# Kernel optimization log

Hardware: AMD Instinct MI355X
Metric: run time of the kernel (lower is better)

Reference implementation:

```python
import jax, jax.numpy as jnp
import numpy as np

B = 8192
DIM = 1024
NI = 16
ALPHA = 0.5
BETA = 1.0


def setup_inputs() -> dict:
    key = jax.random.key(0)
    ks = jax.random.split(key, 12)
    d, n = DIM, NI
    din = d + d // n  # local expert input width = 1088
    s = 0.02  # small init scale to keep softplus in a sane range
    return {
        "y": jax.random.normal(ks[0], (B, d), jnp.float32),
        "M": jax.random.normal(ks[1], (B, d), jnp.float32),
        # global discriminator params ([in, out] layout)
        "gw0": jax.random.normal(ks[2], (d, d), jnp.float32) * s,
        "gb0": jnp.zeros((d,), jnp.float32),
        "gw1": jax.random.normal(ks[3], (d, d), jnp.float32) * s,
        "gb1": jnp.zeros((d,), jnp.float32),
        "l0w": jax.random.normal(ks[4], (2 * d, 128), jnp.float32) * s,
        "l0b": jnp.zeros((128,), jnp.float32),
        "l1w": jax.random.normal(ks[5], (128, 128), jnp.float32) * s,
        "l1b": jnp.zeros((128,), jnp.float32),
        "l2w": jax.random.normal(ks[6], (128, 1), jnp.float32) * s,
        "l2b": jnp.zeros((1,), jnp.float32),
        # local discriminator: n_interpretator stacked expert MLPs
        "lW1": jax.random.normal(ks[7], (n, din, 128), jnp.float32) * s,
        "lb1": jnp.zeros((n, 128), jnp.float32),
        "lW2": jax.random.normal(ks[8], (n, 128, 128), jnp.float32) * s,
        "lb2": jnp.zeros((n, 128), jnp.float32),
        "lW3": jax.random.normal(ks[9], (n, 128, 1), jnp.float32) * s,
        "lb3": jnp.zeros((n, 1), jnp.float32),
        "n_interpretator": NI,
    }


def reference(y, M, gw0, gb0, gw1, gb1, l0w, l0b, l1w, l1b, l2w, l2b,
              lW1, lb1, lW2, lb2, lW3, lb3, n_interpretator):
    n = n_interpretator
    Bsz, d = y.shape
    M3 = M.reshape(Bsz, d // n, n)                              # [B, d/n, n]
    Mp3 = jnp.concatenate([M3[1:], M3[:1]], axis=0)             # shuffled negatives
    y_exp = jnp.broadcast_to(y[:, :, None], (Bsz, d, n))        # [B, d, n]
    yM = jnp.concatenate([M3, y_exp], axis=1)                   # [B, d/n + d, n]
    yMp = jnp.concatenate([Mp3, y_exp], axis=1)

    def local_d(x):
        # batched over the n expert groups: grouped GEMMs instead of a loop
        h = jax.nn.relu(jnp.einsum('bdn,ndh->bnh', x, lW1) + lb1)   # [B, n, 128]
        h = jax.nn.relu(jnp.einsum('bnh,nhk->bnk', h, lW2) + lb2)   # [B, n, 128]
        s = jnp.einsum('bnh,nho->bno', h, lW3) + lb3                # [B, n, 1]
        return s[..., 0]                                            # [B, n]

    Ej_l = -jnp.mean(jax.nn.softplus(-local_d(yM)))
    Em_l = jnp.mean(jax.nn.softplus(local_d(yMp)))
    LOCAL = (Em_l - Ej_l) * BETA

    def global_d(yy, Mm):
        h = jax.nn.relu(Mm.reshape(Bsz, -1) @ gw0 + gb0) @ gw1 + gb1  # net(M)
        h = jnp.concatenate([yy, h], axis=1)                          # [B, 2d]
        h = jax.nn.relu(h @ l0w + l0b)
        h = jax.nn.relu(h @ l1w + l1b)
        return h @ l2w + l2b                                          # [B, 1]

    Ej_g = -jnp.mean(jax.nn.softplus(-global_d(y, M3)))
    Em_g = jnp.mean(jax.nn.softplus(global_d(y, Mp3)))
    GLOBAL = (Em_g - Ej_g) * ALPHA

    return LOCAL + GLOBAL
```

## Files before the change

kernel.cpp:

```cpp
#include <hip/hip_runtime.h>
#include <hip/hip_bf16.h>
#include <math.h>

#define B_ROWS 8192
#define NEXP 16

typedef __attribute__((ext_vector_type(8))) short short8;
typedef __attribute__((ext_vector_type(4))) float f32x4;

__device__ __forceinline__ float softplus_f(float x) {
    return fmaxf(x, 0.f) + log1pf(expf(-fabsf(x)));
}

__device__ __forceinline__ float bf2f(short u) {
    union { unsigned int i; float f; } c;
    c.i = ((unsigned int)(unsigned short)u) << 16;
    return c.f;
}

__device__ __forceinline__ short f2bf_s(float x) {
    __hip_bfloat16 h = __float2bfloat16(x);
    return *(short*)&h;
}

__device__ __forceinline__ void gll16(const void* g, void* l) {
    __builtin_amdgcn_global_load_lds(
        (const __attribute__((address_space(1))) void*)g,
        (__attribute__((address_space(3))) void*)l, 16, 0, 0);
}

#define FENCE() asm volatile("" ::: "memory")
#define VM3 asm volatile("s_waitcnt vmcnt(3)" ::: "memory")
#define VM0 asm volatile("s_waitcnt vmcnt(0)" ::: "memory")
#define BAR __builtin_amdgcn_s_barrier()

__global__ __launch_bounds__(256) void prep_all(
    const float* __restrict__ y, const float* __restrict__ M,
    const float* __restrict__ lW1, const float* __restrict__ gw0,
    const float* __restrict__ l0w, const float* __restrict__ gw1,
    __hip_bfloat16* __restrict__ yb, short* __restrict__ Mt2,
    __hip_bfloat16* __restrict__ W1yt, short* __restrict__ W1m2,
    __hip_bfloat16* __restrict__ W0p, __hip_bfloat16* __restrict__ l0wyt,
    float* __restrict__ wgtp)
{
    __shared__ __align__(16) char smem[33280];
    const int b = blockIdx.x;
    const int tid = threadIdx.x;
    const int lane = tid & 63, w = tid >> 6;

    if (b < 64) {
        short* As = (short*)smem;
        short* Bs = (short*)(smem + 16384);
        const int ct = b & 7, ks = b >> 3;
        const int bn = ct * 128;
        const int wr = w >> 1, wc = w & 1;
        const int l15 = lane & 15, l4 = lane >> 4;

        f32x4 acc4[4][4] = {};
        for (int kq = 0; kq < 2; ++kq) {
            const int k0 = ks * 128 + kq * 64;
            {
                int c4 = (tid & 31) * 4;
                int kkr0 = tid >> 5;
                #pragma unroll
                for (int r = 0; r < 8; ++r) {
                    int kk = r * 8 + kkr0;
                    float4 v = *(const float4*)&l0w[(long)(1024 + k0 + kk) * 128 + c4];
                    int g = kk >> 3, sub = kk & 7;
                    #pragma unroll
                    for (int i = 0; i < 4; ++i) {
                        int row = c4 + i;
                        As[row * 64 + (g ^ (row & 7)) * 8 + sub] = f2bf_s(((const float*)&v)[i]);
                    }
                }
            }
            {
                int jr0 = tid >> 3;
                int g = tid & 7;
                #pragma unroll
                for (int s = 0; s < 4; ++s) {
                    int jrel = s * 32 + jr0;
                    const float* src = &gw1[(long)(bn + jrel) * 1024 + k0 + g * 8];
                    float4 v0 = *(const float4*)src;
                    float4 v1 = *(const float4*)(src + 4);
                    union { short8 v; short sh[8]; } o;
                    o.sh[0] = f2bf_s(v0.x); o.sh[1] = f2bf_s(v0.y);
                    o.sh[2] = f2bf_s(v0.z); o.sh[3] = f2bf_s(v0.w);
                    o.sh[4] = f2bf_s(v1.x); o.sh[5] = f2bf_s(v1.y);
                    o.sh[6] = f2bf_s(v1.z); o.sh[7] = f2bf_s(v1.w);
                    *(short8*)&Bs[jrel * 64 + (g ^ (jrel & 7)) * 8] = o.v;
                }
            }
            __syncthreads();
            #pragma unroll
            for (int st = 0; st < 2; ++st) {
                const int gr = (st * 4 + l4) ^ (l15 & 7);
                short8 a[4], bv[4];
                #pragma unroll
                for (int m = 0; m < 4; ++m)
                    a[m] = *(const short8*)&As[(wr * 64 + m * 16 + l15) * 64 + gr * 8];
                #pragma unroll
                for (int n = 0; n < 4; ++n)
                    bv[n] = *(const short8*)&Bs[(wc * 64 + n * 16 + l15) * 64 + gr * 8];
                #pragma unroll
                for (int m = 0; m < 4; ++m)
                    #pragma unroll
                    for (int n = 0; n < 4; ++n)
                        acc4[m][n] = __builtin_amdgcn_mfma_f32_16x16x32_bf16(a[m], bv[n], acc4[m][n], 0, 0, 0);
            }
            __syncthreads();
        }
        #pragma unroll
        for (int m = 0; m < 4; ++m) {
            int row = wr * 64 + m * 16 + l4 * 4;
            #pragma unroll
            for (int n = 0; n < 4; ++n) {
                int col = bn + wc * 64 + n * 16 + l15;
                #pragma unroll
                for (int r = 0; r < 4; ++r)
                    wgtp[((long)ks * 128 + row + r) * 1024 + col] = acc4[m][n][r];
            }
        }
        return;
    }

    if (b < 1088) {
        const long base = (long)(b - 64) * 2048;
        #pragma unroll
        for (int j = 0; j < 8; ++j) {
            long i = base + j * 256 + tid;
            float4 v = ((const float4*)y)[i];
            union { ushort4 u; __hip_bfloat16 h[4]; } p;
            p.h[0] = __float2bfloat16(v.x);
            p.h[1] = __float2bfloat16(v.y);
            p.h[2] = __float2bfloat16(v.z);
            p.h[3] = __float2bfloat16(v.w);
            ((ushort4*)yb)[i] = p.u;
        }
        return;
    }

    if (b < 2112) {
        short* t = (short*)smem;
        const long r0 = (long)(b - 1088) * 8;
        #pragma unroll
        for (int i = 0; i < 8; ++i) {
            int idx = i * 1024 + tid * 4;
            float4 v = *(const float4*)&M[r0 * 1024 + idx];
            short4 s;
            s.x = f2bf_s(v.x); s.y = f2bf_s(v.y); s.z = f2bf_s(v.z); s.w = f2bf_s(v.w);
            *(short4*)&t[idx] = s;
        }
        __syncthreads();
        const int e = tid & 15, rr = (tid >> 4) & 7, hf = tid >> 7;
        #pragma unroll
        for (int c = 0; c < 4; ++c) {
            union { short8 v; short s[8]; } o;
            #pragma unroll
            for (int j = 0; j < 8; ++j)
                o.s[j] = t[rr * 1024 + (hf * 32 + c * 8 + j) * 16 + e];
            *(short8*)&Mt2[(long)(e >> 1) * (8192L * 128) + (r0 + rr) * 128
                           + (e & 1) * 64 + hf * 32 + c * 8] = o.v;
        }
        return;
    }

    float (*t)[129] = (float(*)[129])smem;

    if (b < 2624) {
        int l = b - 2112, bx = l & 15, by = l >> 4;
        int n0 = bx * 128, k0 = by * 32;
        long base = 64L * 128 + (long)bx * (1088L * 128);
        #pragma unroll
        for (int ll = 0; ll < 16; ++ll) {
            int idx = tid + ll * 256;
            int kk = idx >> 7, nn = idx & 127;
            t[kk][nn] = lW1[base + (long)(k0 + kk) * 128 + nn];
        }
        __syncthreads();
        int nn = tid >> 1, kb = (tid & 1) * 16;
        #pragma unroll
        for (int j = 0; j < 16; ++j)
            W1yt[(long)(n0 + nn) * 1024 + k0 + kb + j] = __float2bfloat16(t[kb + j][nn]);
        return;
    }

    if (b < 2656) {
        int l = b - 2624, bx = l & 15, by = l >> 4;
        int n0 = bx * 128, k0 = by * 32;
        long base = (long)bx * (1088L * 128);
        #pragma unroll
        for (int ll = 0; ll < 16; ++ll) {
            int idx = tid + ll * 256;
            int kk = idx >> 7, nn = idx & 127;
            if (kk < 32) t[kk][nn] = lW1[base + (long)(k0 + kk) * 128 + nn];
        }
        __syncthreads();
        int nn = tid >> 1, kb = (tid & 1) * 16;
        int half = bx & 1;
        #pragma unroll
        for (int j = 0; j < 16; ++j) {
            W1m2[(long)(n0 + nn) * 128 + half * 64 + k0 + kb + j] = f2bf_s(t[kb + j][nn]);
            W1m2[(long)(n0 + nn) * 128 + (1 - half) * 64 + k0 + kb + j] = 0;
        }
        return;
    }

    if (b < 2912) {
        int l = b - 2656, bx = l & 7, by = l >> 3;
        int n0 = bx * 128, k0 = by * 32;
        int e = k0 >> 6, dd0 = k0 & 63;
        #pragma unroll
        for (int ll = 0; ll < 16; ++ll) {
            int idx = tid + ll * 256;
            int kk = idx >> 7, nn = idx & 127;
            t[kk][nn] = gw0[(long)((dd0 + kk) * 16 + e) * 1024 + n0 + nn];
        }
        __syncthreads();
        int nn = tid >> 1, kb = (tid & 1) * 16;
        #pragma unroll
        for (int j = 0; j < 16; ++j)
            W0p[(long)(n0 + nn) * 1024 + k0 + kb + j] = __float2bfloat16(t[kb + j][nn]);
        return;
    }

    {
        int by = b - 2912;
        int k0 = by * 32;
        #pragma unroll
        for (int ll = 0; ll < 16; ++ll) {
            int idx = tid + ll * 256;
            int kk = idx >> 7, nn = idx & 127;
            t[kk][nn] = l0w[(long)(k0 + kk) * 128 + nn];
        }
        __syncthreads();
        int nn = tid >> 1, kb = (tid & 1) * 16;
        #pragma unroll
        for (int j = 0; j < 16; ++j)
            l0wyt[(long)nn * 1024 + k0 + kb + j] = __float2bfloat16(t[kb + j][nn]);
        return;
    }
}

__global__ __launch_bounds__(512, 4) void gemm3s(
    const short* __restrict__ yb, const short* __restrict__ W1yt,
    __hip_bfloat16* __restrict__ Y1b,
    const short* __restrict__ Mt2, const short* __restrict__ W1m2,
    __hip_bfloat16* __restrict__ Mpb,
    const short* __restrict__ W0p, const float* __restrict__ gb0,
    __hip_bfloat16* __restrict__ H0b,
    const float* __restrict__ wgtp, __hip_bfloat16* __restrict__ WgTb,
    const float* __restrict__ l0w, const float* __restrict__ l0b,
    const float* __restrict__ gb1, const float* __restrict__ lW2,
    const float* __restrict__ l1w, float* __restrict__ bing,
    short* __restrict__ W2sb, short* __restrict__ L1ws,
    double* __restrict__ acc_g, int* __restrict__ counter)
{
    __shared__ __align__(16) char smem[49152];
    const int tid = threadIdx.x;
    const int lane = tid & 63, w = tid >> 6;
    const int l15 = lane & 15, l4 = lane >> 4;
    const int wr = w >> 2, wc = w & 3;

    const int bid = blockIdx.x;

    if (bid >= 768 && bid < 794) {
        const int a = bid - 768;
        if (a < 8) {
            #pragma unroll
            for (int j = 0; j < 8; ++j) {
                int i4 = tid + j * 512;
                int flat = i4 * 4;
                int row = flat >> 7, cc = flat & 127;
                const long base = (long)row * 1024 + a * 128 + cc;
                f32x4 s = {};
                #pragma unroll
                for (int ks = 0; ks < 8; ++ks) {
                    f32x4 v = *(const f32x4*)&wgtp[(long)ks * 131072 + base];
                    s += v;
                }
                union { ushort4 u; __hip_bfloat16 h[4]; } o;
                o.h[0] = __float2bfloat16(s[0]);
                o.h[1] = __float2bfloat16(s[1]);
                o.h[2] = __float2bfloat16(s[2]);
                o.h[3] = __float2bfloat16(s[3]);
                *(ushort4*)&WgTb[base] = o.u;
            }
            return;
        }
        if (a == 8) {
            float* part = (float*)smem;
            const int c = tid & 127, q = tid >> 7;
            float s = (q == 0) ? l0b[c] : 0.f;
            const float* p = l0w + (long)(1024 + q * 256) * 128 + c;
            const float* g = gb1 + q * 256;
            #pragma unroll 8
            for (int o = 0; o < 256; ++o)
                s = fmaf(g[o], p[(long)o * 128], s);
            part[tid] = s;
            __syncthreads();
            if (tid < 128)
                bing[tid] = part[tid] + part[tid + 128]
                          + part[tid + 256] + part[tid + 384];
            if (tid == 511) { acc_g[0] = 0.0; acc_g[1] = 0.0; *counter = 0; }
            return;
        }
        {
            int bb = a - 9;
            const float* in = (bb < 16) ? lW2 + (long)bb * 16384 : l1w;
            short* out = (bb < 16) ? W2sb + (long)bb * 16384 : L1ws;
            float (*t2)[65] = (float(*)[65])smem;
            #pragma unroll
            for (int h = 0; h < 2; ++h) {
                if (h) __syncthreads();
                #pragma unroll
                for (int l = 0; l < 16; ++l) {
                    int idx = l * 512 + tid;
                    int kk = idx >> 6, cc = idx & 63;
                    t2[kk][cc] = in[(long)kk * 128 + h * 64 + cc];
                }
                __syncthreads();
                #pragma unroll
                for (int l = 0; l < 2; ++l) {
                    int c2 = l * 512 + tid;
                    int col = h * 64 + (c2 >> 4), kc = c2 & 15;
                    int kcs = kc ^ (col & 7);
                    union { short8 v; short s[8]; } u;
                    #pragma unroll
                    for (int j = 0; j < 8; ++j)
                        u.s[j] = f2bf_s(t2[kc * 8 + j][col - h * 64]);
                    *(short8*)&out[col * 128 + kcs * 8] = u.v;
                }
            }
            return;
        }
    }

    int grp, bm, bn, K;
    const short* A; const short* Wt; __hip_bfloat16* C; int ldc;
    if (bid < 768) {
        const int xcd = bid & 7;
        const int idx = bid >> 3;
        if (idx < 64) {
            grp = 0; const int c = idx >> 3, r = idx & 7;
            bm = (xcd * 8 + r) * 128; bn = c * 256;
            A = yb; Wt = W1yt + (long)bn * 1024; K = 1024; C = Y1b; ldc = 2048;
        } else {
            int j = idx - 64; const int c = j >> 3, r = j & 7;
            grp = 2; bm = (xcd * 8 + r) * 128; bn = c * 256;
            A = Mt2; Wt = W0p + (long)bn * 1024; K = 1024; C = H0b; ldc = 1024;
        }
    } else {
        int j = bid - 794;
        const int xcd = j & 7;
        const int jj = j >> 3;
        const int c = jj >> 3, r = jj & 7;
        grp = 1; bm = (xcd * 8 + r) * 128; bn = c * 256;
        A = Mt2 + (long)(bn >> 8) * (8192L * 128);
        Wt = W1m2 + (long)bn * 128; K = 128; C = Mpb; ldc = 2048;
    }
    const int nt = K >> 5;

    const int rowA = tid >> 2;
    const int sgA  = (tid & 3) ^ ((rowA >> 1) & 3);
    const int rowB0 = tid >> 2;
    const int sgB0  = (tid & 3) ^ ((rowB0 >> 1) & 3);
    const int rowB1 = (tid + 512) >> 2;
    const int sgB1  = (tid & 3) ^ ((rowB1 >> 1) & 3);

    auto STAGE = [&](int t, int sl) {
        char* base = smem + sl * 24576;
        const short* asrc;
        if (grp == 2) {
            const int g = t * 4 + sgA;
            asrc = A + (long)(g >> 4) * (8192L * 128)
                     + (long)(bm + rowA) * 128 + (g & 15) * 8;
        } else {
            asrc = A + (long)(bm + rowA) * K + t * 32 + sgA * 8;
        }
        gll16(asrc, base + w * 1024);
        gll16(Wt + (long)rowB0 * K + t * 32 + sgB0 * 8,
              base + 8192 + w * 1024);
        gll16(Wt + (long)rowB1 * K + t * 32 + sgB1 * 8,
              base + 16384 + w * 1024);
    };

    f32x4 acc[4][4] = {};
    const int xr = (l4 ^ ((l15 >> 1) & 3)) * 16;
    const int aOff = (wr * 64 + l15) * 64 + xr;
    const int bOff = 8192 + (wc * 64 + l15) * 64 + xr;

    auto COMPUTE = [&](int sl) {
        const char* base = smem + sl * 24576;
        short8 a_[4], b_[4];
        #pragma unroll
        for (int m = 0; m < 4; ++m)
            a_[m] = *(const short8*)(base + aOff + m * 1024);
        #pragma unroll
        for (int n = 0; n < 4; ++n)
            b_[n] = *(const short8*)(base + bOff + n * 1024);
        __builtin_amdgcn_s_setprio(1);
        #pragma unroll
        for (int m = 0; m < 4; ++m)
            #pragma unroll
            for (int n = 0; n < 4; ++n)
                acc[m][n] = __builtin_amdgcn_mfma_f32_16x16x32_bf16(
                    a_[m], b_[n], acc[m][n], 0, 0, 0);
        __builtin_amdgcn_s_setprio(0);
    };

    STAGE(0, 0);
    STAGE(1, 1);
    VM3; FENCE(); BAR; FENCE();

    for (int t = 0; t < nt; ++t) {
        COMPUTE(t & 1);
        FENCE(); BAR; FENCE();
        if (t + 2 < nt) {
            STAGE(t + 2, t & 1);
            VM3;
            FENCE(); BAR; FENCE();
        } else if (t == nt - 2) {
            VM0;
            FENCE(); BAR; FENCE();
        }
    }

    #pragma unroll
    for (int m = 0; m < 4; ++m) {
        const int row = bm + wr * 64 + m * 16 + l4 * 4;
        #pragma unroll
        for (int n = 0; n < 4; ++n) {
            const int col = bn + wc * 64 + n * 16 + l15;
            const float bv = (grp == 2) ? gb0[col] : 0.f;
            #pragma unroll
            for (int r = 0; r < 4; ++r) {
                float v = acc[m][n][r] + bv;
                if (grp == 2) v = fmaxf(v, 0.f);
                C[(long)(row + r) * ldc + col] = __float2bfloat16(v);
            }
        }
    }
}

__global__ __launch_bounds__(256) void tail_plus(
    const __hip_bfloat16* __restrict__ Yp, const __hip_bfloat16* __restrict__ Mq,
    const float* __restrict__ bin, const short* __restrict__ W2s,
    const float* __restrict__ b2, const float* __restrict__ w3,
    const float* __restrict__ b3, double* __restrict__ acc,
    const short* __restrict__ H0b, const short* __restrict__ WgTb,
    __hip_bfloat16* __restrict__ Tgb,
    const short* __restrict__ ybs, const short* __restrict__ l0ws,
    __hip_bfloat16* __restrict__ Tyb)
{
    __shared__ __align__(16) char smem[35328];
    const int bid = blockIdx.x;
    const int tid = threadIdx.x;
    const int lane = tid & 63;
    const int l15 = lane & 15, l4 = lane >> 4;

    if (bid >= 2048) {
        const int sel = bid - 2048;
        const short* Ain = (sel < 64) ? H0b : ybs;
        const short* Bin = (sel < 64) ? WgTb : l0ws;
        __hip_bfloat16* Co = (sel < 64) ? Tgb : Tyb;
        short* As = (short*)smem;
        short* Bs = (short*)(smem + 16384);
        const int w = tid >> 6;
        const int wr = w >> 1, wc = w & 1;
        const int bm = (sel & 63) * 128;
        const int srow = lane >> 3;
        const int gsrc = (lane & 7) ^ srow;

        f32x4 a4[4][4] = {};
        for (int k0 = 0; k0 < 1024; k0 += 64) {
            #pragma unroll
            for (int s = 0; s < 4; ++s) {
                const int rrel = s * 32 + w * 8 + srow;
                gll16(Ain + (long)(bm + rrel) * 1024 + k0 + gsrc * 8,
                      As + (s * 32 + w * 8) * 64);
                gll16(Bin + (long)rrel * 1024 + k0 + gsrc * 8,
                      Bs + (s * 32 + w * 8) * 64);
            }
            __syncthreads();
            #pragma unroll
            for (int st = 0; st < 2; ++st) {
                const int gr = (st * 4 + l4) ^ (l15 & 7);
                short8 a[4], b[4];
                #pragma unroll
                for (int m = 0; m < 4; ++m)
                    a[m] = *(const short8*)&As[(wr * 64 + m * 16 + l15) * 64 + gr * 8];
                #pragma unroll
                for (int n = 0; n < 4; ++n)
                    b[n] = *(const short8*)&Bs[(wc * 64 + n * 16 + l15) * 64 + gr * 8];
                #pragma unroll
                for (int m = 0; m < 4; ++m)
                    #pragma unroll
                    for (int n = 0; n < 4; ++n)
                        a4[m][n] = __builtin_amdgcn_mfma_f32_16x16x32_bf16(a[m], b[n], a4[m][n], 0, 0, 0);
            }
            __syncthreads();
        }
        #pragma unroll
        for (int m = 0; m < 4; ++m) {
            int row = bm + (w >> 1) * 64 + m * 16 + l4 * 4;
            #pragma unroll
            for (int n = 0; n < 4; ++n) {
                int col = (w & 1) * 64 + n * 16 + l15;
                #pragma unroll
                for (int r = 0; r < 4; ++r)
                    Co[(long)(row + r) * 128 + col] = __float2bfloat16(a4[m][n][r]);
            }
        }
        return;
    }

    const int wkid = (bid & 7) * 256 + (bid >> 3);
    const int e = wkid & 15;
    const int b0 = (wkid >> 4) * 64;
    const int cbase = e * 128;
    const int wid = tid >> 6;
    const int side = wid >> 1;
    const int wr = wid & 1;
    const int widthIn = 2048;

    short* h1 = (short*)smem;
    float* bins = (float*)(smem + 32768);
    float* b2s  = (float*)(smem + 33280);
    float* w3s  = (float*)(smem + 33792);
    float* red  = (float*)(smem + 34304);

    const short* W2e = W2s + (long)e * 16384;
    if (tid < 128) {
        bins[tid] = bin[cbase + tid];
        b2s[tid]  = b2[cbase + tid];
        w3s[tid]  = w3[cbase + tid];
    }
    __syncthreads();

    const short* Ys = (const short*)Yp;
    const short* Ms = (const short*)Mq;
    #pragma unroll
    for (int c = 0; c < 4; ++c) {
        int chunk = c * 256 + tid;
        int row = chunk >> 4, kc = chunk & 15;
        short8 yv = *(const short8*)&Ys[(long)(b0 + row) * widthIn + cbase + kc * 8];
        float yf[8];
        #pragma unroll
        for (int j = 0; j < 8; ++j) yf[j] = bf2f(yv[j]) + bins[kc * 8 + j];
        int dst = row * 128 + (kc ^ (row & 7)) * 8;
        #pragma unroll
        for (int s = 0; s < 2; ++s) {
            int rowm = (b0 + row + s) & (B_ROWS - 1);
            short8 mv = *(const short8*)&Ms[(long)rowm * widthIn + cbase + kc * 8];
            union { short8 v; short sh[8]; } o;
            #pragma unroll
            for (int j = 0; j < 8; ++j)
                o.sh[j] = f2bf_s(fmaxf(yf[j] + bf2f(mv[j]), 0.f));
            *(short8*)&h1[s * 8192 + dst] = o.v;
        }
    }
    __syncthreads();

    f32x4 accv[2][8] = {};
    #pragma unroll
    for (int st = 0; st < 4; ++st) {
        short8 a[2], b[8];
        #pragma unroll
        for (int m = 0; m < 2; ++m) {
            int row = wr * 32 + m * 16 + l15;
            int ch = (st * 4 + l4) ^ (row & 7);
            a[m] = *(const short8*)&h1[side * 8192 + row * 128 + ch * 8];
        }
        #pragma unroll
        for (int n = 0; n < 8; ++n) {
            int col = n * 16 + l15;
            int ch = (st * 4 + l4) ^ (col & 7);
            b[n] = *(const short8*)&W2e[col * 128 + ch * 8];
        }
        #pragma unroll
        for (int m = 0; m < 2; ++m)
            #pragma unroll
            for (int n = 0; n < 8; ++n)
                accv[m][n] = __builtin_amdgcn_mfma_f32_16x16x32_bf16(a[m], b[n], accv[m][n], 0, 0, 0);
    }

    float p[2][4] = {};
    #pragma unroll
    for (int m = 0; m < 2; ++m)
        #pragma unroll
        for (int n = 0; n < 8; ++n) {
            int colL = n * 16 + l15;
            float bb = b2s[colL], ww = w3s[colL];
            #pragma unroll
            for (int r = 0; r < 4; ++r) {
                float h2 = fmaxf(accv[m][n][r] + bb, 0.f);
                p[m][r] = fmaf(h2, ww, p[m][r]);
            }
        }
    #pragma unroll
    for (int m = 0; m < 2; ++m)
        #pragma unroll
        for (int r = 0; r < 4; ++r)
            #pragma unroll
            for (int off = 1; off < 16; off <<= 1)
                p[m][r] += __shfl_xor(p[m][r], off, 64);

    float mysum = 0.f;
    if (l15 == 0) {
        float bb = b3[e];
        #pragma unroll
        for (int m = 0; m < 2; ++m)
            #pragma unroll
            for (int r = 0; r < 4; ++r) {
                float s = p[m][r] + bb;
                mysum += softplus_f(side ? s : -s);
            }
    }
    red[tid] = mysum;
    __syncthreads();
    for (int s2 = 128; s2 > 0; s2 >>= 1) {
        if (tid < s2) red[tid] += red[tid + s2];
        __syncthreads();
    }
    if (tid == 0) atomicAdd(acc, (double)red[0]);
}

__global__ __launch_bounds__(256) void tail_mfma(
    const __hip_bfloat16* __restrict__ Yp, const __hip_bfloat16* __restrict__ Mq,
    const float* __restrict__ bin,
    const short* __restrict__ W2s,
    const float* __restrict__ b2, const float* __restrict__ w3,
    const float* __restrict__ b3,
    int widthIn, double* __restrict__ acc, int* __restrict__ counter,
    float* __restrict__ out)
{
    const int b0 = blockIdx.x * 64;
    const int e = blockIdx.y;
    const int cbase = e * 128;
    const int tid = threadIdx.x;
    const int lane = tid & 63;
    const int wid = tid >> 6;
    const int side = wid >> 1;
    const int wr = wid & 1;

    __shared__ __align__(16) short h1[2 * 64 * 128];
    __shared__ __align__(16) short Bs[128 * 128];
    __shared__ float bins[128], b2s[128], w3s[128];
    __shared__ float red[256];

    const short* W2e = W2s + (long)e * 16384;
    #pragma unroll
    for (int l = 0; l < 8; ++l) {
        int cb = (l * 4 + wid) * 64;
        gll16(W2e + (long)(cb + lane) * 8, &Bs[cb * 8]);
    }
    if (tid < 128) {
        bins[tid] = bin[cbase + tid];
        b2s[tid]  = b2[cbase + tid];
        w3s[tid]  = w3[cbase + tid];
    }
    __syncthreads();

    const short* Ys = (const short*)Yp;
    const short* Ms = (const short*)Mq;
    #pragma unroll
    for (int c = 0; c < 4; ++c) {
        int chunk = c * 256 + tid;
        int row = chunk >> 4, kc = chunk & 15;
        short8 yv = *(const short8*)&Ys[(long)(b0 + row) * widthIn + cbase + kc * 8];
        float yf[8];
        #pragma unroll
        for (int j = 0; j < 8; ++j) yf[j] = bf2f(yv[j]) + bins[kc * 8 + j];
        int dst = row * 128 + (kc ^ (row & 7)) * 8;
        #pragma unroll
        for (int s = 0; s < 2; ++s) {
            int rowm = (b0 + row + s) & (B_ROWS - 1);
            short8 mv = *(const short8*)&Ms[(long)rowm * widthIn + cbase + kc * 8];
            union { short8 v; short sh[8]; } o;
            #pragma unroll
            for (int j = 0; j < 8; ++j)
                o.sh[j] = f2bf_s(fmaxf(yf[j] + bf2f(mv[j]), 0.f));
            *(short8*)&h1[s * 8192 + dst] = o.v;
        }
    }
    __syncthreads();

    const int l15 = lane & 15, l4 = lane >> 4;
    f32x4 accv[2][8] = {};
    #pragma unroll
    for (int st = 0; st < 4; ++st) {
        short8 a[2], b[8];
        #pragma unroll
        for (int m = 0; m < 2; ++m) {
            int row = wr * 32 + m * 16 + l15;
            int ch = (st * 4 + l4) ^ (row & 7);
            a[m] = *(const short8*)&h1[side * 8192 + row * 128 + ch * 8];
        }
        #pragma unroll
        for (int n = 0; n < 8; ++n) {
            int col = n * 16 + l15;
            int ch = (st * 4 + l4) ^ (col & 7);
            b[n] = *(const short8*)&Bs[col * 128 + ch * 8];
        }
        #pragma unroll
        for (int m = 0; m < 2; ++m)
            #pragma unroll
            for (int n = 0; n < 8; ++n)
                accv[m][n] = __builtin_amdgcn_mfma_f32_16x16x32_bf16(a[m], b[n], accv[m][n], 0, 0, 0);
    }

    float p[2][4] = {};
    #pragma unroll
    for (int m = 0; m < 2; ++m)
        #pragma unroll
        for (int n = 0; n < 8; ++n) {
            int colL = n * 16 + l15;
            float bb = b2s[colL], ww = w3s[colL];
            #pragma unroll
            for (int r = 0; r < 4; ++r) {
                float h2 = fmaxf(accv[m][n][r] + bb, 0.f);
                p[m][r] = fmaf(h2, ww, p[m][r]);
            }
        }
    #pragma unroll
    for (int m = 0; m < 2; ++m)
        #pragma unroll
        for (int r = 0; r < 4; ++r)
            #pragma unroll
            for (int off = 1; off < 16; off <<= 1)
                p[m][r] += __shfl_xor(p[m][r], off, 64);

    float mysum = 0.f;
    if (l15 == 0) {
        float bb = b3[e];
        #pragma unroll
        for (int m = 0; m < 2; ++m)
            #pragma unroll
            for (int r = 0; r < 4; ++r) {
                float s = p[m][r] + bb;
                mysum += softplus_f(side ? s : -s);
            }
    }
    red[tid] = mysum;
    __syncthreads();
    for (int s2 = 128; s2 > 0; s2 >>= 1) {
        if (tid < s2) red[tid] += red[tid + s2];
        __syncthreads();
    }
    if (tid == 0) {
        atomicAdd(acc + 1, (double)red[0]);
        __threadfence();
        int old = atomicAdd(counter, 1);
        if (old == (int)(gridDim.x * gridDim.y) - 1) {
            double a0 = atomicAdd(acc + 0, 0.0);
            double a1 = atomicAdd(acc + 1, 0.0);
            out[0] = (float)(a0 / (8192.0 * 16.0) + 0.5 * a1 / 8192.0);
        }
    }
}

extern "C" void kernel_launch(void* const* d_in, const int* in_sizes, int n_in,
                              void* d_out, int out_size, void* d_ws, size_t ws_size,
                              hipStream_t stream)
{
    const float* y   = (const float*)d_in[0];
    const float* M   = (const float*)d_in[1];
    const float* gw0 = (const float*)d_in[2];
    const float* gb0 = (const float*)d_in[3];
    const float* gw1 = (const float*)d_in[4];
    const float* gb1 = (const float*)d_in[5];
    const float* l0w = (const float*)d_in[6];
    const float* l0b = (const float*)d_in[7];
    const float* l1w = (const float*)d_in[8];
    const float* l1b = (const float*)d_in[9];
    const float* l2w = (const float*)d_in[10];
    const float* l2b = (const float*)d_in[11];
    const float* lW1 = (const float*)d_in[12];
    const float* lb1 = (const float*)d_in[13];
    const float* lW2 = (const float*)d_in[14];
    const float* lb2 = (const float*)d_in[15];
    const float* lW3 = (const float*)d_in[16];
    const float* lb3 = (const float*)d_in[17];

    char* w = (char*)d_ws;
    double* acc = (double*)w;
    int* counter = (int*)(w + 16);
    float* bing = (float*)(w + 256);
    const size_t MB = 1u << 20;
    __hip_bfloat16* Y1b  = (__hip_bfloat16*)(w + 4096);
    __hip_bfloat16* Mpb  = (__hip_bfloat16*)(w + 4096 + 32 * MB);
    __hip_bfloat16* H0b  = (__hip_bfloat16*)(w + 4096 + 64 * MB);
    short*          Mt2  = (short*)(w + 4096 + 80 * MB);
    __hip_bfloat16* yb   = (__hip_bfloat16*)(w + 4096 + 96 * MB);
    __hip_bfloat16* W1yt = (__hip_bfloat16*)(w + 4096 + 112 * MB);
    __hip_bfloat16* W0p  = (__hip_bfloat16*)(w + 4096 + 118 * MB);
    __hip_bfloat16* l0wyt = (__hip_bfloat16*)(w + 4096 + 120 * MB);
    short* W2sb = (short*)(w + 4096 + 120 * MB + 512 * 1024);
    short* L1ws = (short*)(w + 4096 + 121 * MB);
    __hip_bfloat16* WgTb = (__hip_bfloat16*)(w + 4096 + 121 * MB + 512 * 1024);
    short* W1m2 = (short*)(w + 4096 + 122 * MB);
    __hip_bfloat16* Tyb = (__hip_bfloat16*)(w + 4096 + 123 * MB);
    __hip_bfloat16* Tgb = (__hip_bfloat16*)(w + 4096 + 125 * MB);
    float* wgtp = (float*)(w + 4096 + 123 * MB);

    dim3 blk(256);

    prep_all<<<dim3(2944), blk, 0, stream>>>(
        y, M, lW1, gw0, l0w, gw1,
        yb, Mt2, W1yt, W1m2, W0p, l0wyt, wgtp);

    gemm3s<<<dim3(1306), dim3(512), 0, stream>>>(
        (const short*)yb, (const short*)W1yt, Y1b,
        Mt2, W1m2, Mpb,
        (const short*)W0p, gb0, H0b,
        wgtp, WgTb,
        l0w, l0b, gb1, lW2, l1w, bing, W2sb, L1ws,
        acc, counter);

    tail_plus<<<dim3(2176), blk, 0, stream>>>(
        Y1b, Mpb, lb1, W2sb, lb2, lW3, lb3, acc,
        (const short*)H0b, (const short*)WgTb, Tgb,
        (const short*)yb, (const short*)l0wyt, Tyb);

    tail_mfma<<<dim3(128, 1), blk, 0, stream>>>(
        Tyb, Tgb, bing, L1ws, l1b, l2w, l2b, 128, acc, counter,
        (float*)d_out);
}
```

Measured before the change: 170.6 us.

## Split global GEMM out of tail_plus and halve its LDS footprint

The two 128-block global-discriminator GEMMs that were folded into tail_plus move into a separate tailG kernel. tail_plus then handles the positive and negative sides one after another using a single 16 KB h1 buffer instead of two. Each wave now takes a 16-row tile and sweeps the columns in two halves, and launch bounds of 8 blocks per SM are requested. This is meant to cut LDS use and registers so more blocks fit per CU. The cost is an extra kernel launch and serialized side processing with more barriers.

New measurement: 402.1 us. +135.6%, slower.

```diff
diff --git a/kernel.cpp b/kernel.cpp
--- a/kernel.cpp
+++ b/kernel.cpp
@@ -443,92 +443,95 @@
     }
 }
 
-__global__ __launch_bounds__(256) void tail_plus(
-    const __hip_bfloat16* __restrict__ Yp, const __hip_bfloat16* __restrict__ Mq,
-    const float* __restrict__ bin, const short* __restrict__ W2s,
-    const float* __restrict__ b2, const float* __restrict__ w3,
-    const float* __restrict__ b3, double* __restrict__ acc,
+__global__ __launch_bounds__(256) void tailG(
     const short* __restrict__ H0b, const short* __restrict__ WgTb,
     __hip_bfloat16* __restrict__ Tgb,
     const short* __restrict__ ybs, const short* __restrict__ l0ws,
     __hip_bfloat16* __restrict__ Tyb)
 {
-    __shared__ __align__(16) char smem[35328];
+    __shared__ __align__(16) char smem[32768];
+    const int sel = blockIdx.x;
+    const int tid = threadIdx.x;
+    const int lane = tid & 63;
+    const int l15 = lane & 15, l4 = lane >> 4;
+
+    const short* Ain = (sel < 64) ? H0b : ybs;
+    const short* Bin = (sel < 64) ? WgTb : l0ws;
+    __hip_bfloat16* Co = (sel < 64) ? Tgb : Tyb;
+    short* As = (short*)smem;
+    short* Bs = (short*)(smem + 16384);
+    const int w = tid >> 6;
+    const int wr = w >> 1, wc = w & 1;
+    const int bm = (sel & 63) * 128;
+    const int srow = lane >> 3;
+    const int gsrc = (lane & 7) ^ srow;
+
+    f32x4 a4[4][4] = {};
+    for (int k0 = 0; k0 < 1024; k0 += 64) {
+        #pragma unroll
+        for (int s = 0; s < 4; ++s) {
+            const int rrel = s * 32 + w * 8 + srow;
+            gll16(Ain + (long)(bm + rrel) * 1024 + k0 + gsrc * 8,
+                  As + (s * 32 + w * 8) * 64);
+            gll16(Bin + (long)rrel * 1024 + k0 + gsrc * 8,
+                  Bs + (s * 32 + w * 8) * 64);
+        }
+        __syncthreads();
+        #pragma unroll
+        for (int st = 0; st < 2; ++st) {
+            const int gr = (st * 4 + l4) ^ (l15 & 7);
+            short8 a[4], b[4];
+            #pragma unroll
+            for (int m = 0; m < 4; ++m)
+                a[m] = *(const short8*)&As[(wr * 64 + m * 16 + l15) * 64 + gr * 8];
+            #pragma unroll
+            for (int n = 0; n < 4; ++n)
+                b[n] = *(const short8*)&Bs[(wc * 64 + n * 16 + l15) * 64 + gr * 8];
+            #pragma unroll
+            for (int m = 0; m < 4; ++m)
+                #pragma unroll
+                for (int n = 0; n < 4; ++n)
+                    a4[m][n] = __builtin_amdgcn_mfma_f32_16x16x32_bf16(a[m], b[n], a4[m][n], 0, 0, 0);
+        }
+        __syncthreads();
+    }
+    #pragma unroll
+    for (int m = 0; m < 4; ++m) {
+        int row = bm + (w >> 1) * 64 + m * 16 + l4 * 4;
+        #pragma unroll
+        for (int n = 0; n < 4; ++n) {
+            int col = (w & 1) * 64 + n * 16 + l15;
+            #pragma unroll
+            for (int r = 0; r < 4; ++r)
+                Co[(long)(row + r) * 128 + col] = __float2bfloat16(a4[m][n][r]);
+        }
+    }
+}
+
+__global__ __launch_bounds__(256, 8) void tail_plus(
+    const __hip_bfloat16* __restrict__ Yp, const __hip_bfloat16* __restrict__ Mq,
+    const float* __restrict__ bin, const short* __restrict__ W2s,
+    const float* __restrict__ b2, const float* __restrict__ w3,
+    const float* __restrict__ b3, double* __restrict__ acc)
+{
+    __shared__ __align__(16) char smem[18944];
     const int bid = blockIdx.x;
     const int tid = threadIdx.x;
     const int lane = tid & 63;
     const int l15 = lane & 15, l4 = lane >> 4;
-
-    if (bid >= 2048) {
-        const int sel = bid - 2048;
-        const short* Ain = (sel < 64) ? H0b : ybs;
-        const short* Bin = (sel < 64) ? WgTb : l0ws;
-        __hip_bfloat16* Co = (sel < 64) ? Tgb : Tyb;
-        short* As = (short*)smem;
-        short* Bs = (short*)(smem + 16384);
-        const int w = tid >> 6;
-        const int wr = w >> 1, wc = w & 1;
-        const int bm = (sel & 63) * 128;
-        const int srow = lane >> 3;
-        const int gsrc = (lane & 7) ^ srow;
-
-        f32x4 a4[4][4] = {};
-        for (int k0 = 0; k0 < 1024; k0 += 64) {
-            #pragma unroll
-            for (int s = 0; s < 4; ++s) {
-                const int rrel = s * 32 + w * 8 + srow;
-                gll16(Ain + (long)(bm + rrel) * 1024 + k0 + gsrc * 8,
-                      As + (s * 32 + w * 8) * 64);
-                gll16(Bin + (long)rrel * 1024 + k0 + gsrc * 8,
-                      Bs + (s * 32 + w * 8) * 64);
-            }
-            __syncthreads();
-            #pragma unroll
-            for (int st = 0; st < 2; ++st) {
-                const int gr = (st * 4 + l4) ^ (l15 & 7);
-                short8 a[4], b[4];
-                #pragma unroll
-                for (int m = 0; m < 4; ++m)
-                    a[m] = *(const short8*)&As[(wr * 64 + m * 16 + l15) * 64 + gr * 8];
-                #pragma unroll
-                for (int n = 0; n < 4; ++n)
-                    b[n] = *(const short8*)&Bs[(wc * 64 + n * 16 + l15) * 64 + gr * 8];
-                #pragma unroll
-                for (int m = 0; m < 4; ++m)
-                    #pragma unroll
-                    for (int n = 0; n < 4; ++n)
-                        a4[m][n] = __builtin_amdgcn_mfma_f32_16x16x32_bf16(a[m], b[n], a4[m][n], 0, 0, 0);
-            }
-            __syncthreads();
-        }
-        #pragma unroll
-        for (int m = 0; m < 4; ++m) {
-            int row = bm + (w >> 1) * 64 + m * 16 + l4 * 4;
-            #pragma unroll
-            for (int n = 0; n < 4; ++n) {
-                int col = (w & 1) * 64 + n * 16 + l15;
-                #pragma unroll
-                for (int r = 0; r < 4; ++r)
-                    Co[(long)(row + r) * 128 + col] = __float2bfloat16(a4[m][n][r]);
-            }
-        }
-        return;
-    }
+    const int wid = tid >> 6;
 
     const int wkid = (bid & 7) * 256 + (bid >> 3);
     const int e = wkid & 15;
     const int b0 = (wkid >> 4) * 64;
     const int cbase = e * 128;
-    const int wid = tid >> 6;
-    const int side = wid >> 1;
-    const int wr = wid & 1;
     const int widthIn = 2048;
 
     short* h1 = (short*)smem;
-    float* bins = (float*)(smem + 32768);
-    float* b2s  = (float*)(smem + 33280);
-    float* w3s  = (float*)(smem + 33792);
-    float* red  = (float*)(smem + 34304);
+    float* bins = (float*)(smem + 16384);
+    float* b2s  = (float*)(smem + 16896);
+    float* w3s  = (float*)(smem + 17408);
+    float* red  = (float*)(smem + 17920);
 
     const short* W2e = W2s + (long)e * 16384;
     if (tid < 128) {
@@ -540,83 +543,69 @@
 
     const short* Ys = (const short*)Yp;
     const short* Ms = (const short*)Mq;
-    #pragma unroll
-    for (int c = 0; c < 4; ++c) {
-        int chunk = c * 256 + tid;
-        int row = chunk >> 4, kc = chunk & 15;
-        short8 yv = *(const short8*)&Ys[(long)(b0 + row) * widthIn + cbase + kc * 8];
-        float yf[8];
-        #pragma unroll
-        for (int j = 0; j < 8; ++j) yf[j] = bf2f(yv[j]) + bins[kc * 8 + j];
-        int dst = row * 128 + (kc ^ (row & 7)) * 8;
-        #pragma unroll
-        for (int s = 0; s < 2; ++s) {
+    const float bb3 = b3[e];
+
+    float mysum = 0.f;
+
+    for (int s = 0; s < 2; ++s) {
+        #pragma unroll
+        for (int c = 0; c < 4; ++c) {
+            int chunk = c * 256 + tid;
+            int row = chunk >> 4, kc = chunk & 15;
+            short8 yv = *(const short8*)&Ys[(long)(b0 + row) * widthIn + cbase + kc * 8];
             int rowm = (b0 + row + s) & (B_ROWS - 1);
             short8 mv = *(const short8*)&Ms[(long)rowm * widthIn + cbase + kc * 8];
             union { short8 v; short sh[8]; } o;
             #pragma unroll
             for (int j = 0; j < 8; ++j)
-                o.sh[j] = f2bf_s(fmaxf(yf[j] + bf2f(mv[j]), 0.f));
-            *(short8*)&h1[s * 8192 + dst] = o.v;
-        }
-    }
-    __syncthreads();
-
-    f32x4 accv[2][8] = {};
-    #pragma unroll
-    for (int st = 0; st < 4; ++st) {
-        short8 a[2], b[8];
-        #pragma unroll
-        for (int m = 0; m < 2; ++m) {
-            int row = wr * 32 + m * 16 + l15;
-            int ch = (st * 4 + l4) ^ (row & 7);
-            a[m] = *(const short8*)&h1[side * 8192 + row * 128 + ch * 8];
-        }
-        #pragma unroll
-        for (int n = 0; n < 8; ++n) {
-            int col = n * 16 + l15;
-            int ch = (st * 4 + l4) ^ (col & 7);
-            b[n] = *(const short8*)&W2e[col * 128 + ch * 8];
-        }
-        #pragma unroll
-        for (int m = 0; m < 2; ++m)
-            #pragma unroll
-            for (int n = 0; n < 8; ++n)
-                accv[m][n] = __builtin_amdgcn_mfma_f32_16x16x32_bf16(a[m], b[n], accv[m][n], 0, 0, 0);
-    }
-
-    float p[2][4] = {};
-    #pragma unroll
-    for (int m = 0; m < 2; ++m)
-        #pragma unroll
-        for (int n = 0; n < 8; ++n) {
-            int colL = n * 16 + l15;
-            float bb = b2s[colL], ww = w3s[colL];
+                o.sh[j] = f2bf_s(fmaxf(bf2f(yv[j]) + bins[kc * 8 + j] + bf2f(mv[j]), 0.f));
+            *(short8*)&h1[row * 128 + (kc ^ (row & 7)) * 8] = o.v;
+        }
+        __syncthreads();
+
+        float pr[4] = {0.f, 0.f, 0.f, 0.f};
+        #pragma unroll
+        for (int cp = 0; cp < 2; ++cp) {
+            f32x4 accv[4] = {};
+            #pragma unroll
+            for (int st = 0; st < 4; ++st) {
+                const int arow = wid * 16 + l15;
+                const int ch = (st * 4 + l4) ^ (arow & 7);
+                short8 a = *(const short8*)&h1[arow * 128 + ch * 8];
+                #pragma unroll
+                for (int n = 0; n < 4; ++n) {
+                    const int col = cp * 64 + n * 16 + l15;
+                    const int ch2 = (st * 4 + l4) ^ (col & 7);
+                    short8 b = *(const short8*)&W2e[col * 128 + ch2 * 8];
+                    accv[n] = __builtin_amdgcn_mfma_f32_16x16x32_bf16(a, b, accv[n], 0, 0, 0);
+                }
+            }
+            #pragma unroll
+            for (int n = 0; n < 4; ++n) {
+                const int colL = cp * 64 + n * 16 + l15;
+                const float bb = b2s[colL], ww = w3s[colL];
+                #pragma unroll
+                for (int r = 0; r < 4; ++r) {
+                    float h2 = fmaxf(accv[n][r] + bb, 0.f);
+                    pr[r] = fmaf(h2, ww, pr[r]);
+                }
+            }
+        }
+        #pragma unroll
+        for (int r = 0; r < 4; ++r)
+            #pragma unroll
+            for (int off = 1; off < 16; off <<= 1)
+                pr[r] += __shfl_xor(pr[r], off, 64);
+        if (l15 == 0) {
             #pragma unroll
             for (int r = 0; r < 4; ++r) {
-                float h2 = fmaxf(accv[m][n][r] + bb, 0.f);
-                p[m][r] = fmaf(h2, ww, p[m][r]);
-            }
-        }
-    #pragma unroll
-    for (int m = 0; m < 2; ++m)
-        #pragma unroll
-        for (int r = 0; r < 4; ++r)
-            #pragma unroll
-            for (int off = 1; off < 16; off <<= 1)
-                p[m][r] += __shfl_xor(p[m][r], off, 64);
-
-    float mysum = 0.f;
-    if (l15 == 0) {
-        float bb = b3[e];
-        #pragma unroll
-        for (int m = 0; m < 2; ++m)
-            #pragma unroll
-            for (int r = 0; r < 4; ++r) {
-                float s = p[m][r] + bb;
-                mysum += softplus_f(side ? s : -s);
-            }
-    }
+                float sc = pr[r] + bb3;
+                mysum += softplus_f(s ? sc : -sc);
+            }
+        }
+        __syncthreads();
+    }
+
     red[tid] = mysum;
     __syncthreads();
     for (int s2 = 128; s2 > 0; s2 >>= 1) {
@@ -818,10 +807,12 @@
         l0w, l0b, gb1, lW2, l1w, bing, W2sb, L1ws,
         acc, counter);
 
-    tail_plus<<<dim3(2176), blk, 0, stream>>>(
-        Y1b, Mpb, lb1, W2sb, lb2, lW3, lb3, acc,
+    tailG<<<dim3(128), blk, 0, stream>>>(
         (const short*)H0b, (const short*)WgTb, Tgb,
         (const short*)yb, (const short*)l0wyt, Tyb);
+
+    tail_plus<<<dim3(2048), blk, 0, stream>>>(
+        Y1b, Mpb, lb1, W2sb, lb2, lW3, lb3, acc);
 
     tail_mfma<<<dim3(128, 1), blk, 0, stream>>>(
         Tyb, Tgb, bing, L1ws, l1b, l2w, l2b, 128, acc, counter,
```
